# Kernel optimization log

Hardware: AMD Instinct MI355X
Metric: run time of the kernel (lower is better)

Reference implementation:

```python
import jax, jax.numpy as jnp
import numpy as np

V, C, E = 100000, 50000, 1250000
VF, CF, H = 32, 32, 64
ROUNDS = 3


def setup_inputs() -> dict:
    key = jax.random.key(0)
    ks = jax.random.split(key, 16)
    s = lambda d: 1.0 / np.sqrt(d)
    inp = {
        "var_feat": jax.random.normal(ks[0], (V, VF), dtype=jnp.float32),
        "constr_feat": jax.random.normal(ks[1], (C, CF), dtype=jnp.float32),
        "W_var": jax.random.uniform(ks[2], (VF, H), jnp.float32, -s(VF), s(VF)),
        "b_var": jax.random.uniform(ks[3], (H,), jnp.float32, -s(VF), s(VF)),
        "W_con": jax.random.uniform(ks[4], (CF, H), jnp.float32, -s(CF), s(CF)),
        "b_con": jax.random.uniform(ks[5], (H,), jnp.float32, -s(CF), s(CF)),
        "W_v2c": jax.random.uniform(ks[6], (H, H), jnp.float32, -s(H), s(H)),
        "b_v2c": jax.random.uniform(ks[7], (H,), jnp.float32, -s(H), s(H)),
        "W_c2v": jax.random.uniform(ks[8], (H, H), jnp.float32, -s(H), s(H)),
        "b_c2v": jax.random.uniform(ks[9], (H,), jnp.float32, -s(H), s(H)),
        "W_score": jax.random.uniform(ks[10], (H, 1), jnp.float32, -s(H), s(H)),
        "b_score": jax.random.uniform(ks[11], (1,), jnp.float32, -s(H), s(H)),
        "var_idx": jax.random.randint(ks[12], (E,), 0, V, dtype=jnp.int64 if jax.config.jax_enable_x64 else jnp.int32),
        "constr_idx": jax.random.randint(ks[13], (E,), 0, C, dtype=jnp.int64 if jax.config.jax_enable_x64 else jnp.int32),
    }
    return inp


def reference(var_feat, constr_feat, W_var, b_var, W_con, b_con, W_v2c, b_v2c,
              W_c2v, b_c2v, W_score, b_score, var_idx, constr_idx):
    nV = var_feat.shape[0]
    nC = constr_feat.shape[0]
    h_var = jax.nn.relu(var_feat @ W_var + b_var)          # [V, H]
    h_constr = jax.nn.relu(constr_feat @ W_con + b_con)    # [C, H]
    for _ in range(ROUNDS):
        # gather var states along edges, scatter-add into constraint buffer
        msg_c = jax.ops.segment_sum(h_var[var_idx], constr_idx, num_segments=nC)  # [C, H]
        h_constr = jax.nn.relu(h_constr + msg_c @ W_v2c + b_v2c)
        # gather constraint states along edges, scatter-add into variable buffer
        msg_v = jax.ops.segment_sum(h_constr[constr_idx], var_idx, num_segments=nV)  # [V, H]
        h_var = jax.nn.relu(h_var + msg_v @ W_c2v + b_c2v)
    scores = (h_var @ W_score + b_score).reshape(-1)       # [V]
    return scores
```

## Files before the change

kernel.cpp:

```cpp
#include <hip/hip_runtime.h>

typedef unsigned short u16;
typedef unsigned int u32;
typedef __attribute__((ext_vector_type(8))) short short8v;
typedef __attribute__((ext_vector_type(4))) float f32x4;

#define V_N 100000
#define C_N 50000
#define E_N 1250000
#define VF_N 32
#define H_N 64
#define ROUNDS 3

#define TILE 4096
#define NT ((E_N + TILE - 1) / TILE)
#define NB_C ((C_N + 127) / 128)
#define NB_V ((V_N + 255) / 256)
#define FC_BLOCKS 768
#define KPAD 72

static __device__ __forceinline__ float bf2f(u16 x) {
  return __uint_as_float(((u32)x) << 16);
}
static __device__ __forceinline__ u16 f2bf(float f) {
  u32 u = __float_as_uint(f);
  u32 r = (u + 0x7fff + ((u >> 16) & 1)) >> 16;
  return (u16)r;
}


__global__ __launch_bounds__(256) void bucket_hist(const int* __restrict__ vi,
                                                   const int* __restrict__ ci,
                                                   int* __restrict__ gh_c,
                                                   int* __restrict__ gh_v) {
  __shared__ int hc[NB_C], hv[NB_V];
  int t = threadIdx.x;
  for (int j = t; j < NB_C; j += 256) hc[j] = 0;
  for (int j = t; j < NB_V; j += 256) hv[j] = 0;
  __syncthreads();
  int base = blockIdx.x * TILE;
#pragma unroll
  for (int i = 0; i < 16; ++i) {
    int idx = base + i * 256 + t;
    if (idx < E_N) {
      atomicAdd(&hc[ci[idx] >> 7], 1);
      atomicAdd(&hv[vi[idx] >> 8], 1);
    }
  }
  __syncthreads();
  for (int j = t; j < NB_C; j += 256) if (hc[j]) atomicAdd(&gh_c[j], hc[j]);
  for (int j = t; j < NB_V; j += 256) if (hv[j]) atomicAdd(&gh_v[j], hv[j]);
}

__global__ __launch_bounds__(512) void bucket_scan(const int* __restrict__ gh_c,
                                                   const int* __restrict__ gh_v,
                                                   int* __restrict__ base_c,
                                                   int* __restrict__ cursor_c,
                                                   int* __restrict__ base_v,
                                                   int* __restrict__ cursor_v,
                                                   int* __restrict__ rs_c,
                                                   int* __restrict__ rs_v) {
  __shared__ int lds[512];
  int t = threadIdx.x;
  int x = (t < NB_C) ? gh_c[t] : 0;
  lds[t] = x;
  __syncthreads();
  for (int off = 1; off < 512; off <<= 1) {
    int v = (t >= off) ? lds[t - off] : 0;
    __syncthreads();
    lds[t] += v;
    __syncthreads();
  }
  int excl = lds[t] - x;
  if (t < NB_C) { base_c[t] = excl; cursor_c[t] = excl; }
  if (t == 511) base_c[NB_C] = lds[511];
  __syncthreads();
  int y = (t < NB_V) ? gh_v[t] : 0;
  lds[t] = y;
  __syncthreads();
  for (int off = 1; off < 512; off <<= 1) {
    int v = (t >= off) ? lds[t - off] : 0;
    __syncthreads();
    lds[t] += v;
    __syncthreads();
  }
  int excl2 = lds[t] - y;
  if (t < NB_V) { base_v[t] = excl2; cursor_v[t] = excl2; }
  if (t == 511) base_v[NB_V] = lds[511];
  if (t == 0) { rs_c[C_N] = E_N; rs_v[V_N] = E_N; }
}

__global__ __launch_bounds__(256) void scatter_pack(const int* __restrict__ vi,
                                                    const int* __restrict__ ci,
                                                    int* __restrict__ cursor_c,
                                                    int* __restrict__ cursor_v,
                                                    int* __restrict__ packed_c,
                                                    int* __restrict__ packed_v) {
  __shared__ int hc[NB_C], hv[NB_V], sc[NB_C], sv[NB_V];
  int t = threadIdx.x;
  for (int j = t; j < NB_C; j += 256) hc[j] = 0;
  for (int j = t; j < NB_V; j += 256) hv[j] = 0;
  __syncthreads();
  int base = blockIdx.x * TILE;
  int cc[16], vv[16];
#pragma unroll
  for (int i = 0; i < 16; ++i) {
    int idx = base + i * 256 + t;
    if (idx < E_N) {
      cc[i] = ci[idx];
      vv[i] = vi[idx];
      atomicAdd(&hc[cc[i] >> 7], 1);
      atomicAdd(&hv[vv[i] >> 8], 1);
    } else {
      cc[i] = -1;
      vv[i] = -1;
    }
  }
  __syncthreads();
  for (int j = t; j < NB_C; j += 256) {
    int n = hc[j];
    if (n > 0) sc[j] = atomicAdd(&cursor_c[j], n);
    hc[j] = 0;
  }
  for (int j = t; j < NB_V; j += 256) {
    int n = hv[j];
    if (n > 0) sv[j] = atomicAdd(&cursor_v[j], n);
    hv[j] = 0;
  }
  __syncthreads();
#pragma unroll
  for (int i = 0; i < 16; ++i) {
    if (cc[i] >= 0) {
      int b = cc[i] >> 7;
      int r = atomicAdd(&hc[b], 1);
      packed_c[sc[b] + r] = ((cc[i] & 127) << 17) | vv[i];
      int b2 = vv[i] >> 8;
      int r2 = atomicAdd(&hv[b2], 1);
      packed_v[sv[b2] + r2] = ((vv[i] & 255) << 17) | cc[i];
    }
  }
}

template <int LOCAL_N, int N_DEST>
__global__ __launch_bounds__(256) void fine_sort(const int* __restrict__ packed,
                                                 const int* __restrict__ base,
                                                 int* __restrict__ rs,
                                                 int* __restrict__ srco) {
  __shared__ int cnt[LOCAL_N];
  __shared__ int excl[LOCAL_N];
  int b = blockIdx.x, t = threadIdx.x;
  int s0 = base[b], s1 = base[b + 1];
  if (t < LOCAL_N) cnt[t] = 0;
  __syncthreads();
  for (int i = s0 + t; i < s1; i += 256) atomicAdd(&cnt[packed[i] >> 17], 1);
  __syncthreads();
  if (t == 0) {
    int run = 0;
    for (int k = 0; k < LOCAL_N; ++k) { excl[k] = run; run += cnt[k]; }
  }
  __syncthreads();
  if (t < LOCAL_N) {
    int d = b * LOCAL_N + t;
    if (d < N_DEST) rs[d] = s0 + excl[t];
    cnt[t] = excl[t];
  }
  __syncthreads();
  for (int i = s0 + t; i < s1; i += 256) {
    int w = packed[i];
    int ld = w >> 17;
    int pos = s0 + atomicAdd(&cnt[ld], 1);
    srco[pos] = w & 0x1FFFF;
  }
}


__global__ __launch_bounds__(256) void prep_w(const float* __restrict__ W1,
                                              const float* __restrict__ W2,
                                              u16* __restrict__ wp) {
  int i = blockIdx.x * 256 + threadIdx.x;
  if (i >= H_N * H_N) return;
  int k = i >> 6, n = i & 63;
  float w1 = W1[i];
  u16 h1 = f2bf(w1);
  u16 l1 = f2bf(w1 - bf2f(h1));
  wp[(0 * 64 + n) * 64 + k] = h1;
  wp[(1 * 64 + n) * 64 + k] = l1;
  float w2 = W2[i];
  u16 h2 = f2bf(w2);
  u16 l2 = f2bf(w2 - bf2f(h2));
  wp[(2 * 64 + n) * 64 + k] = h2;
  wp[(3 * 64 + n) * 64 + k] = l2;
}


template <int WRITE_BF>
__global__ __launch_bounds__(256) void init_mlp(const float* __restrict__ feat,
                                                const float* __restrict__ W,
                                                const float* __restrict__ b,
                                                float* __restrict__ h,
                                                u16* __restrict__ hbf, int n) {
  __shared__ float Wl[VF_N * H_N];
  for (int i = threadIdx.x; i < VF_N * H_N; i += 256) Wl[i] = W[i];
  __syncthreads();
  int g = (blockIdx.x * 256 + threadIdx.x) >> 4;
  int lane = threadIdx.x & 15;
  if (g >= n) return;
  float2 rv = *(const float2*)&feat[(size_t)g * VF_N + lane * 2];
  float4 acc = *(const float4*)&b[lane * 4];
#pragma unroll
  for (int k = 0; k < VF_N; ++k) {
    float el = (k & 1) ? rv.y : rv.x;
    float v = __shfl(el, k >> 1, 16);
    float4 w = *(const float4*)&Wl[k * H_N + lane * 4];
    acc.x += v * w.x; acc.y += v * w.y; acc.z += v * w.z; acc.w += v * w.w;
  }
  acc.x = fmaxf(acc.x, 0.f); acc.y = fmaxf(acc.y, 0.f);
  acc.z = fmaxf(acc.z, 0.f); acc.w = fmaxf(acc.w, 0.f);
  *(float4*)&h[(size_t)g * H_N + lane * 4] = acc;
  if (WRITE_BF) {
    ushort4 q;
    q.x = f2bf(acc.x); q.y = f2bf(acc.y); q.z = f2bf(acc.z); q.w = f2bf(acc.w);
    *(ushort4*)&hbf[(size_t)g * H_N + lane * 4] = q;
  }
}


static __device__ __forceinline__ void gather_rows_bf16(const u16* __restrict__ tbl,
                                                        const int* __restrict__ src,
                                                        int s, int e, int lane,
                                                        float4& acc) {
  int p = s;
  for (; p + 16 <= e; p += 16) {
    int myidx = src[p + lane];
    ushort4 vv[16];
#pragma unroll
    for (int j = 0; j < 16; ++j) {
      int sj = __shfl(myidx, j, 16);
      vv[j] = *(const ushort4*)&tbl[(size_t)sj * H_N + lane * 4];
    }
#pragma unroll
    for (int j = 0; j < 16; ++j) {
      acc.x += bf2f(vv[j].x); acc.y += bf2f(vv[j].y);
      acc.z += bf2f(vv[j].z); acc.w += bf2f(vv[j].w);
    }
  }
  if (p < e) {
    int cnt = e - p;
    int myidx = (lane < cnt) ? src[p + lane] : 0;
    ushort4 vv[16];
#pragma unroll
    for (int j = 0; j < 16; ++j) {
      int sj = __shfl(myidx, j, 16);
      vv[j] = *(const ushort4*)&tbl[(size_t)sj * H_N + lane * 4];
    }
#pragma unroll
    for (int j = 0; j < 16; ++j) {
      if (j < cnt) {
        acc.x += bf2f(vv[j].x); acc.y += bf2f(vv[j].y);
        acc.z += bf2f(vv[j].z); acc.w += bf2f(vv[j].w);
      }
    }
  }
}


__global__ __launch_bounds__(256) void fused_c(const u16* __restrict__ h_var_bf,
                                               const int* __restrict__ rs,
                                               const int* __restrict__ src,
                                               const u16* __restrict__ wp,
                                               const float* __restrict__ b1g,
                                               float* __restrict__ h_con,
                                               u16* __restrict__ t_out) {
  __shared__ u16 Wlds[4 * 64 * 64];
  __shared__ u16 Aplanes[4][2 * 16 * KPAD];

  for (int i = threadIdx.x; i < 4 * 64 * 64 / 2; i += 256)
    ((u32*)Wlds)[i] = ((const u32*)wp)[i];
  __syncthreads();

  int lane64 = threadIdx.x & 63;
  int wave = threadIdx.x >> 6;
  int lane = threadIdx.x & 15;
  int grp = (threadIdx.x >> 4) & 3;
  int arow = lane64 & 15;
  int kq = lane64 >> 4;
  u16* P = &Aplanes[wave][0];

  float bias[4];
#pragma unroll
  for (int nt = 0; nt < 4; ++nt) bias[nt] = b1g[nt * 16 + arow];

  for (int base = (blockIdx.x * 4 + wave) * 16; base < C_N;
       base += FC_BLOCKS * 4 * 16) {
    for (int q = 0; q < 4; ++q) {
      int row = 4 * q + grp;
      int g = base + row;
      float4 acc = {0.f, 0.f, 0.f, 0.f};
      if (g < C_N) gather_rows_bf16(h_var_bf, src, rs[g], rs[g + 1], lane, acc);
      ushort4 qh, ql;
      qh.x = f2bf(acc.x); ql.x = f2bf(acc.x - bf2f(qh.x));
      qh.y = f2bf(acc.y); ql.y = f2bf(acc.y - bf2f(qh.y));
      qh.z = f2bf(acc.z); ql.z = f2bf(acc.z - bf2f(qh.z));
      qh.w = f2bf(acc.w); ql.w = f2bf(acc.w - bf2f(qh.w));
      *(ushort4*)&P[0 * 16 * KPAD + row * KPAD + lane * 4] = qh;
      *(ushort4*)&P[1 * 16 * KPAD + row * KPAD + lane * 4] = ql;
    }
    asm volatile("" ::: "memory");
    short8v A1h[2], A1l[2];
#pragma unroll
    for (int ks = 0; ks < 2; ++ks) {
      A1h[ks] = *(const short8v*)&P[0 * 16 * KPAD + arow * KPAD + ks * 32 + kq * 8];
      A1l[ks] = *(const short8v*)&P[1 * 16 * KPAD + arow * KPAD + ks * 32 + kq * 8];
    }
    asm volatile("" ::: "memory");
#pragma unroll
    for (int nt = 0; nt < 4; ++nt) {
      int bcol = nt * 16 + arow;
      f32x4 c = {0.f, 0.f, 0.f, 0.f};
#pragma unroll
      for (int ks = 0; ks < 2; ++ks) {
        short8v Bh = *(const short8v*)&Wlds[(0 * 64 + bcol) * 64 + ks * 32 + kq * 8];
        short8v Bl = *(const short8v*)&Wlds[(1 * 64 + bcol) * 64 + ks * 32 + kq * 8];
        c = __builtin_amdgcn_mfma_f32_16x16x32_bf16(A1h[ks], Bh, c, 0, 0, 0);
        c = __builtin_amdgcn_mfma_f32_16x16x32_bf16(A1l[ks], Bh, c, 0, 0, 0);
        c = __builtin_amdgcn_mfma_f32_16x16x32_bf16(A1h[ks], Bl, c, 0, 0, 0);
      }
#pragma unroll
      for (int r = 0; r < 4; ++r) {
        int row = kq * 4 + r;
        int g = base + row;
        float hv = (g < C_N) ? h_con[(size_t)g * H_N + nt * 16 + arow] : 0.f;
        float hn = fmaxf(hv + c[r] + bias[nt], 0.f);
        if (g < C_N) h_con[(size_t)g * H_N + nt * 16 + arow] = hn;
        u16 hi = f2bf(hn);
        u16 lo = f2bf(hn - bf2f(hi));
        P[0 * 16 * KPAD + row * KPAD + nt * 16 + arow] = hi;
        P[1 * 16 * KPAD + row * KPAD + nt * 16 + arow] = lo;
      }
    }
    asm volatile("" ::: "memory");
    short8v A2h[2], A2l[2];
#pragma unroll
    for (int ks = 0; ks < 2; ++ks) {
      A2h[ks] = *(const short8v*)&P[0 * 16 * KPAD + arow * KPAD + ks * 32 + kq * 8];
      A2l[ks] = *(const short8v*)&P[1 * 16 * KPAD + arow * KPAD + ks * 32 + kq * 8];
    }
    asm volatile("" ::: "memory");
#pragma unroll
    for (int nt = 0; nt < 4; ++nt) {
      int bcol = nt * 16 + arow;
      f32x4 c = {0.f, 0.f, 0.f, 0.f};
#pragma unroll
      for (int ks = 0; ks < 2; ++ks) {
        short8v Bh = *(const short8v*)&Wlds[(2 * 64 + bcol) * 64 + ks * 32 + kq * 8];
        short8v Bl = *(const short8v*)&Wlds[(3 * 64 + bcol) * 64 + ks * 32 + kq * 8];
        c = __builtin_amdgcn_mfma_f32_16x16x32_bf16(A2h[ks], Bh, c, 0, 0, 0);
        c = __builtin_amdgcn_mfma_f32_16x16x32_bf16(A2l[ks], Bh, c, 0, 0, 0);
        c = __builtin_amdgcn_mfma_f32_16x16x32_bf16(A2h[ks], Bl, c, 0, 0, 0);
      }
#pragma unroll
      for (int r = 0; r < 4; ++r) {
        int row = kq * 4 + r;
        int g = base + row;
        if (g < C_N) t_out[(size_t)g * H_N + nt * 16 + arow] = f2bf(c[r]);
      }
    }
    asm volatile("" ::: "memory");
  }
}


template <int DO_SCORE>
__global__ __launch_bounds__(256) void gather_v_k(const u16* __restrict__ t,
                                                  const int* __restrict__ rs,
                                                  const int* __restrict__ src,
                                                  const float* __restrict__ bias,
                                                  float* __restrict__ h,
                                                  u16* __restrict__ hbf,
                                                  const float* __restrict__ Ws,
                                                  const float* __restrict__ bs,
                                                  float* __restrict__ out) {
  int g = (blockIdx.x * 256 + threadIdx.x) >> 4;
  int lane = threadIdx.x & 15;
  if (g >= V_N) return;
  int s = rs[g], e = rs[g + 1];
  float4 acc = {0.f, 0.f, 0.f, 0.f};
  gather_rows_bf16(t, src, s, e, lane, acc);
  float4 hv = *(const float4*)&h[(size_t)g * H_N + lane * 4];
  float4 b4 = *(const float4*)&bias[lane * 4];
  float4 hn;
  hn.x = fmaxf(hv.x + acc.x + b4.x, 0.f);
  hn.y = fmaxf(hv.y + acc.y + b4.y, 0.f);
  hn.z = fmaxf(hv.z + acc.z + b4.z, 0.f);
  hn.w = fmaxf(hv.w + acc.w + b4.w, 0.f);
  if (DO_SCORE) {
    float4 w = *(const float4*)&Ws[lane * 4];
    float d = hn.x * w.x + hn.y * w.y + hn.z * w.z + hn.w * w.w;
    d += __shfl_down(d, 8, 16);
    d += __shfl_down(d, 4, 16);
    d += __shfl_down(d, 2, 16);
    d += __shfl_down(d, 1, 16);
    if (lane == 0) out[g] = d + bs[0];
  } else {
    *(float4*)&h[(size_t)g * H_N + lane * 4] = hn;
    ushort4 q;
    q.x = f2bf(hn.x); q.y = f2bf(hn.y); q.z = f2bf(hn.z); q.w = f2bf(hn.w);
    *(ushort4*)&hbf[(size_t)g * H_N + lane * 4] = q;
  }
}


extern "C" void kernel_launch(void* const* d_in, const int* in_sizes, int n_in,
                              void* d_out, int out_size, void* d_ws, size_t ws_size,
                              hipStream_t stream) {
  const float* var_feat = (const float*)d_in[0];
  const float* con_feat = (const float*)d_in[1];
  const float* W_var = (const float*)d_in[2];
  const float* b_var = (const float*)d_in[3];
  const float* W_con = (const float*)d_in[4];
  const float* b_con = (const float*)d_in[5];
  const float* W_v2c = (const float*)d_in[6];
  const float* b_v2c = (const float*)d_in[7];
  const float* W_c2v = (const float*)d_in[8];
  const float* b_c2v = (const float*)d_in[9];
  const float* W_score = (const float*)d_in[10];
  const float* b_score = (const float*)d_in[11];
  const int* var_idx = (const int*)d_in[12];
  const int* constr_idx = (const int*)d_in[13];
  float* out = (float*)d_out;

  char* p = (char*)d_ws;
  auto alloc = [&](size_t bytes) {
    char* r = p;
    p += (bytes + 255) & ~(size_t)255;
    return r;
  };
  float* h_var = (float*)alloc((size_t)V_N * H_N * 4);
  u16* h_var_bf = (u16*)alloc((size_t)V_N * H_N * 2);
  float* h_con = (float*)alloc((size_t)C_N * H_N * 4);
  u16* t_bf = (u16*)alloc((size_t)C_N * H_N * 2);
  u16* wp = (u16*)alloc((size_t)4 * 64 * 64 * 2);
  int* rs_c = (int*)alloc((size_t)(C_N + 1) * 4);
  int* rs_v = (int*)alloc((size_t)(V_N + 1) * 4);
  int* src_c = (int*)alloc((size_t)E_N * 4);
  int* src_v = (int*)alloc((size_t)E_N * 4);
  int* packed_c = (int*)alloc((size_t)E_N * 4);
  int* packed_v = (int*)alloc((size_t)E_N * 4);
  int* ghist_c = (int*)alloc((size_t)NB_C * 4);
  int* ghist_v = (int*)alloc((size_t)NB_V * 4);
  int* base_c = (int*)alloc((size_t)(NB_C + 1) * 4);
  int* base_v = (int*)alloc((size_t)(NB_V + 1) * 4);
  int* cursor_c = (int*)alloc((size_t)NB_C * 4);
  int* cursor_v = (int*)alloc((size_t)NB_V * 4);

  hipMemsetAsync(ghist_c, 0, (size_t)NB_C * 4, stream);
  hipMemsetAsync(ghist_v, 0, (size_t)NB_V * 4, stream);

  bucket_hist<<<NT, 256, 0, stream>>>(var_idx, constr_idx, ghist_c, ghist_v);
  bucket_scan<<<1, 512, 0, stream>>>(ghist_c, ghist_v, base_c, cursor_c,
                                     base_v, cursor_v, rs_c, rs_v);
  scatter_pack<<<NT, 256, 0, stream>>>(var_idx, constr_idx, cursor_c, cursor_v,
                                       packed_c, packed_v);
  fine_sort<128, C_N><<<NB_C, 256, 0, stream>>>(packed_c, base_c, rs_c, src_c);
  fine_sort<256, V_N><<<NB_V, 256, 0, stream>>>(packed_v, base_v, rs_v, src_v);

  prep_w<<<(H_N * H_N + 255) / 256, 256, 0, stream>>>(W_v2c, W_c2v, wp);

  init_mlp<1><<<(V_N + 15) / 16, 256, 0, stream>>>(var_feat, W_var, b_var, h_var, h_var_bf, V_N);
  init_mlp<0><<<(C_N + 15) / 16, 256, 0, stream>>>(con_feat, W_con, b_con, h_con, nullptr, C_N);

  for (int r = 0; r < ROUNDS; ++r) {
    fused_c<<<FC_BLOCKS, 256, 0, stream>>>(h_var_bf, rs_c, src_c, wp,
                                           b_v2c, h_con, t_bf);
    if (r < ROUNDS - 1) {
      gather_v_k<0><<<(V_N + 15) / 16, 256, 0, stream>>>(t_bf, rs_v, src_v, b_c2v, h_var,
                                                         h_var_bf, nullptr, nullptr, nullptr);
    } else {
      gather_v_k<1><<<(V_N + 15) / 16, 256, 0, stream>>>(t_bf, rs_v, src_v, b_c2v, h_var,
                                                         nullptr, W_score, b_score, out);
    }
  }
}
```

Before: 345.2 us.

## Use 16-byte edge gathers and atomic tile scheduling in fused_c

The constraint-side gather now has each 16-lane group fetch two edge rows at once using 16-byte (8 bf16) loads per lane, and the two half-sums are combined with a shuffle. Each wave also takes 16-row tiles from a global atomic counter, one counter per round, instead of a static stride, which balances the uneven edge counts across waves. This gives wider memory transactions and better load balance, at the cost of more registers for the 16 short8 loads and one atomic per tile.

```diff
diff --git a/kernel.cpp b/kernel.cpp
--- a/kernel.cpp
+++ b/kernel.cpp
@@ -18,6 +18,7 @@
 #define NB_V ((V_N + 255) / 256)
 #define FC_BLOCKS 768
 #define KPAD 72
+#define NTILES_C ((C_N + 15) / 16)
 
 static __device__ __forceinline__ float bf2f(u16 x) {
   return __uint_as_float(((u32)x) << 16);
@@ -264,13 +265,47 @@
 }
 
 
+static __device__ __forceinline__ void gather_rows_wide(const u16* __restrict__ tbl,
+                                                        const int* __restrict__ src,
+                                                        int s, int e, int lane,
+                                                        float* acc8) {
+  int half = lane >> 3;
+  int oct = lane & 7;
+  int p = s;
+  for (; p < e; p += 32) {
+    int rem = e - p;
+    int i0 = p + lane, i1 = p + 16 + lane;
+    int s0 = (i0 < e) ? src[i0] : 0;
+    int s1 = (i1 < e) ? src[i1] : 0;
+    short8v vv[16];
+#pragma unroll
+    for (int j = 0; j < 16; ++j) {
+      int re = 2 * j;
+      int ro = 2 * j + 1;
+      int idA = __shfl((re >= 16) ? s1 : s0, re & 15, 16);
+      int idB = __shfl((ro >= 16) ? s1 : s0, ro & 15, 16);
+      int id = half ? idB : idA;
+      vv[j] = *(const short8v*)&tbl[(size_t)id * H_N + oct * 8];
+    }
+#pragma unroll
+    for (int j = 0; j < 16; ++j) {
+      if (2 * j + half < rem) {
+#pragma unroll
+        for (int k = 0; k < 8; ++k) acc8[k] += bf2f((u16)vv[j][k]);
+      }
+    }
+  }
+}
+
+
 __global__ __launch_bounds__(256) void fused_c(const u16* __restrict__ h_var_bf,
                                                const int* __restrict__ rs,
                                                const int* __restrict__ src,
                                                const u16* __restrict__ wp,
                                                const float* __restrict__ b1g,
                                                float* __restrict__ h_con,
-                                               u16* __restrict__ t_out) {
+                                               u16* __restrict__ t_out,
+                                               int* __restrict__ tile_ctr) {
   __shared__ u16 Wlds[4 * 64 * 64];
   __shared__ u16 Aplanes[4][2 * 16 * KPAD];
 
@@ -282,6 +317,8 @@
   int wave = threadIdx.x >> 6;
   int lane = threadIdx.x & 15;
   int grp = (threadIdx.x >> 4) & 3;
+  int half = lane >> 3;
+  int oct = lane & 7;
   int arow = lane64 & 15;
   int kq = lane64 >> 4;
   u16* P = &Aplanes[wave][0];
@@ -290,20 +327,30 @@
 #pragma unroll
   for (int nt = 0; nt < 4; ++nt) bias[nt] = b1g[nt * 16 + arow];
 
-  for (int base = (blockIdx.x * 4 + wave) * 16; base < C_N;
-       base += FC_BLOCKS * 4 * 16) {
+  for (;;) {
+    int tile = 0;
+    if (lane64 == 0) tile = atomicAdd(tile_ctr, 1);
+    tile = __shfl(tile, 0, 64);
+    if (tile >= NTILES_C) break;
+    int base = tile * 16;
     for (int q = 0; q < 4; ++q) {
       int row = 4 * q + grp;
       int g = base + row;
-      float4 acc = {0.f, 0.f, 0.f, 0.f};
-      if (g < C_N) gather_rows_bf16(h_var_bf, src, rs[g], rs[g + 1], lane, acc);
-      ushort4 qh, ql;
-      qh.x = f2bf(acc.x); ql.x = f2bf(acc.x - bf2f(qh.x));
-      qh.y = f2bf(acc.y); ql.y = f2bf(acc.y - bf2f(qh.y));
-      qh.z = f2bf(acc.z); ql.z = f2bf(acc.z - bf2f(qh.z));
-      qh.w = f2bf(acc.w); ql.w = f2bf(acc.w - bf2f(qh.w));
-      *(ushort4*)&P[0 * 16 * KPAD + row * KPAD + lane * 4] = qh;
-      *(ushort4*)&P[1 * 16 * KPAD + row * KPAD + lane * 4] = ql;
+      float acc8[8] = {0.f, 0.f, 0.f, 0.f, 0.f, 0.f, 0.f, 0.f};
+      if (g < C_N) gather_rows_wide(h_var_bf, src, rs[g], rs[g + 1], lane, acc8);
+      short8v hi8, lo8;
+#pragma unroll
+      for (int k = 0; k < 8; ++k) {
+        float full = acc8[k] + __shfl_xor(acc8[k], 8, 16);
+        u16 h = f2bf(full);
+        u16 l = f2bf(full - bf2f(h));
+        hi8[k] = (short)h;
+        lo8[k] = (short)l;
+      }
+      if (half == 0) {
+        *(short8v*)&P[0 * 16 * KPAD + row * KPAD + oct * 8] = hi8;
+        *(short8v*)&P[1 * 16 * KPAD + row * KPAD + oct * 8] = lo8;
+      }
     }
     asm volatile("" ::: "memory");
     short8v A1h[2], A1l[2];
@@ -452,9 +499,11 @@
   int* base_v = (int*)alloc((size_t)(NB_V + 1) * 4);
   int* cursor_c = (int*)alloc((size_t)NB_C * 4);
   int* cursor_v = (int*)alloc((size_t)NB_V * 4);
+  int* tile_ctr = (int*)alloc((size_t)ROUNDS * 4);
 
   hipMemsetAsync(ghist_c, 0, (size_t)NB_C * 4, stream);
   hipMemsetAsync(ghist_v, 0, (size_t)NB_V * 4, stream);
+  hipMemsetAsync(tile_ctr, 0, (size_t)ROUNDS * 4, stream);
 
   bucket_hist<<<NT, 256, 0, stream>>>(var_idx, constr_idx, ghist_c, ghist_v);
   bucket_scan<<<1, 512, 0, stream>>>(ghist_c, ghist_v, base_c, cursor_c,
@@ -471,7 +520,7 @@
 
   for (int r = 0; r < ROUNDS; ++r) {
     fused_c<<<FC_BLOCKS, 256, 0, stream>>>(h_var_bf, rs_c, src_c, wp,
-                                           b_v2c, h_con, t_bf);
+                                           b_v2c, h_con, t_bf, &tile_ctr[r]);
     if (r < ROUNDS - 1) {
       gather_v_k<0><<<(V_N + 15) / 16, 256, 0, stream>>>(t_bf, rs_v, src_v, b_c2v, h_var,
                                                          h_var_bf, nullptr, nullptr, nullptr);
```

Result: slower. 470.1 us (+36.2%).

## Use one tile per wave with 8-wave blocks in fused constraint kernel

Applied to the files above, without the earlier changes.

Replaces the persistent grid-stride loop in fused_c with one 16-row tile per wave, 8 waves per 512-thread block, and a grid sized to cover all tiles. The four row gathers are issued before any conversion so their loads can overlap. The hi and lo bf16 planes now share one LDS buffer per wave and are built one after the other, which halves per-wave LDS for the A planes. This trades the amortized weight-to-LDS load of persistent blocks for more blocks, each reloading the 32KB of weights, in exchange for better load balance and occupancy.

```diff
diff --git a/kernel.cpp b/kernel.cpp
--- a/kernel.cpp
+++ b/kernel.cpp
@@ -16,8 +16,10 @@
 #define NT ((E_N + TILE - 1) / TILE)
 #define NB_C ((C_N + 127) / 128)
 #define NB_V ((V_N + 255) / 256)
-#define FC_BLOCKS 768
 #define KPAD 72
+#define NTILES_C ((C_N + 15) / 16)
+#define FC_WAVES 8
+#define FC_BLOCKS ((NTILES_C + FC_WAVES - 1) / FC_WAVES)
 
 static __device__ __forceinline__ float bf2f(u16 x) {
   return __uint_as_float(((u32)x) << 16);
@@ -264,7 +266,7 @@
 }
 
 
-__global__ __launch_bounds__(256) void fused_c(const u16* __restrict__ h_var_bf,
+__global__ __launch_bounds__(512) void fused_c(const u16* __restrict__ h_var_bf,
                                                const int* __restrict__ rs,
                                                const int* __restrict__ src,
                                                const u16* __restrict__ wp,
@@ -272,9 +274,9 @@
                                                float* __restrict__ h_con,
                                                u16* __restrict__ t_out) {
   __shared__ u16 Wlds[4 * 64 * 64];
-  __shared__ u16 Aplanes[4][2 * 16 * KPAD];
-
-  for (int i = threadIdx.x; i < 4 * 64 * 64 / 2; i += 256)
+  __shared__ u16 Aplane[FC_WAVES][16 * KPAD];
+
+  for (int i = threadIdx.x; i < 4 * 64 * 64 / 2; i += 512)
     ((u32*)Wlds)[i] = ((const u32*)wp)[i];
   __syncthreads();
 
@@ -284,88 +286,120 @@
   int grp = (threadIdx.x >> 4) & 3;
   int arow = lane64 & 15;
   int kq = lane64 >> 4;
-  u16* P = &Aplanes[wave][0];
+  u16* P = &Aplane[wave][0];
+
+  int tile = blockIdx.x * FC_WAVES + wave;
+  if (tile >= NTILES_C) return;
+  int base = tile * 16;
 
   float bias[4];
 #pragma unroll
   for (int nt = 0; nt < 4; ++nt) bias[nt] = b1g[nt * 16 + arow];
 
-  for (int base = (blockIdx.x * 4 + wave) * 16; base < C_N;
-       base += FC_BLOCKS * 4 * 16) {
-    for (int q = 0; q < 4; ++q) {
-      int row = 4 * q + grp;
+  float4 accs[4];
+#pragma unroll
+  for (int q = 0; q < 4; ++q) {
+    int row = 4 * q + grp;
+    int g = base + row;
+    float4 a = {0.f, 0.f, 0.f, 0.f};
+    if (g < C_N) gather_rows_bf16(h_var_bf, src, rs[g], rs[g + 1], lane, a);
+    accs[q] = a;
+  }
+#pragma unroll
+  for (int q = 0; q < 4; ++q) {
+    int row = 4 * q + grp;
+    ushort4 qh;
+    qh.x = f2bf(accs[q].x); qh.y = f2bf(accs[q].y);
+    qh.z = f2bf(accs[q].z); qh.w = f2bf(accs[q].w);
+    *(ushort4*)&P[row * KPAD + lane * 4] = qh;
+  }
+  asm volatile("" ::: "memory");
+  short8v A1h[2];
+#pragma unroll
+  for (int ks = 0; ks < 2; ++ks)
+    A1h[ks] = *(const short8v*)&P[arow * KPAD + ks * 32 + kq * 8];
+  asm volatile("" ::: "memory");
+#pragma unroll
+  for (int q = 0; q < 4; ++q) {
+    int row = 4 * q + grp;
+    ushort4 ql;
+    ql.x = f2bf(accs[q].x - bf2f(f2bf(accs[q].x)));
+    ql.y = f2bf(accs[q].y - bf2f(f2bf(accs[q].y)));
+    ql.z = f2bf(accs[q].z - bf2f(f2bf(accs[q].z)));
+    ql.w = f2bf(accs[q].w - bf2f(f2bf(accs[q].w)));
+    *(ushort4*)&P[row * KPAD + lane * 4] = ql;
+  }
+  asm volatile("" ::: "memory");
+  short8v A1l[2];
+#pragma unroll
+  for (int ks = 0; ks < 2; ++ks)
+    A1l[ks] = *(const short8v*)&P[arow * KPAD + ks * 32 + kq * 8];
+  asm volatile("" ::: "memory");
+  float hn[4][4];
+#pragma unroll
+  for (int nt = 0; nt < 4; ++nt) {
+    int bcol = nt * 16 + arow;
+    f32x4 c = {0.f, 0.f, 0.f, 0.f};
+#pragma unroll
+    for (int ks = 0; ks < 2; ++ks) {
+      short8v Bh = *(const short8v*)&Wlds[(0 * 64 + bcol) * 64 + ks * 32 + kq * 8];
+      short8v Bl = *(const short8v*)&Wlds[(1 * 64 + bcol) * 64 + ks * 32 + kq * 8];
+      c = __builtin_amdgcn_mfma_f32_16x16x32_bf16(A1h[ks], Bh, c, 0, 0, 0);
+      c = __builtin_amdgcn_mfma_f32_16x16x32_bf16(A1l[ks], Bh, c, 0, 0, 0);
+      c = __builtin_amdgcn_mfma_f32_16x16x32_bf16(A1h[ks], Bl, c, 0, 0, 0);
+    }
+#pragma unroll
+    for (int r = 0; r < 4; ++r) {
+      int row = kq * 4 + r;
       int g = base + row;
-      float4 acc = {0.f, 0.f, 0.f, 0.f};
-      if (g < C_N) gather_rows_bf16(h_var_bf, src, rs[g], rs[g + 1], lane, acc);
-      ushort4 qh, ql;
-      qh.x = f2bf(acc.x); ql.x = f2bf(acc.x - bf2f(qh.x));
-      qh.y = f2bf(acc.y); ql.y = f2bf(acc.y - bf2f(qh.y));
-      qh.z = f2bf(acc.z); ql.z = f2bf(acc.z - bf2f(qh.z));
-      qh.w = f2bf(acc.w); ql.w = f2bf(acc.w - bf2f(qh.w));
-      *(ushort4*)&P[0 * 16 * KPAD + row * KPAD + lane * 4] = qh;
-      *(ushort4*)&P[1 * 16 * KPAD + row * KPAD + lane * 4] = ql;
-    }
-    asm volatile("" ::: "memory");
-    short8v A1h[2], A1l[2];
+      float hv = (g < C_N) ? h_con[(size_t)g * H_N + nt * 16 + arow] : 0.f;
+      float v = fmaxf(hv + c[r] + bias[nt], 0.f);
+      if (g < C_N) h_con[(size_t)g * H_N + nt * 16 + arow] = v;
+      hn[nt][r] = v;
+    }
+  }
+#pragma unroll
+  for (int nt = 0; nt < 4; ++nt)
+#pragma unroll
+    for (int r = 0; r < 4; ++r)
+      P[(kq * 4 + r) * KPAD + nt * 16 + arow] = f2bf(hn[nt][r]);
+  asm volatile("" ::: "memory");
+  short8v A2h[2];
+#pragma unroll
+  for (int ks = 0; ks < 2; ++ks)
+    A2h[ks] = *(const short8v*)&P[arow * KPAD + ks * 32 + kq * 8];
+  asm volatile("" ::: "memory");
+#pragma unroll
+  for (int nt = 0; nt < 4; ++nt)
+#pragma unroll
+    for (int r = 0; r < 4; ++r) {
+      u16 hi = f2bf(hn[nt][r]);
+      P[(kq * 4 + r) * KPAD + nt * 16 + arow] = f2bf(hn[nt][r] - bf2f(hi));
+    }
+  asm volatile("" ::: "memory");
+  short8v A2l[2];
+#pragma unroll
+  for (int ks = 0; ks < 2; ++ks)
+    A2l[ks] = *(const short8v*)&P[arow * KPAD + ks * 32 + kq * 8];
+  asm volatile("" ::: "memory");
+#pragma unroll
+  for (int nt = 0; nt < 4; ++nt) {
+    int bcol = nt * 16 + arow;
+    f32x4 c = {0.f, 0.f, 0.f, 0.f};
 #pragma unroll
     for (int ks = 0; ks < 2; ++ks) {
-      A1h[ks] = *(const short8v*)&P[0 * 16 * KPAD + arow * KPAD + ks * 32 + kq * 8];
-      A1l[ks] = *(const short8v*)&P[1 * 16 * KPAD + arow * KPAD + ks * 32 + kq * 8];
-    }
-    asm volatile("" ::: "memory");
-#pragma unroll
-    for (int nt = 0; nt < 4; ++nt) {
-      int bcol = nt * 16 + arow;
-      f32x4 c = {0.f, 0.f, 0.f, 0.f};
-#pragma unroll
-      for (int ks = 0; ks < 2; ++ks) {
-        short8v Bh = *(const short8v*)&Wlds[(0 * 64 + bcol) * 64 + ks * 32 + kq * 8];
-        short8v Bl = *(const short8v*)&Wlds[(1 * 64 + bcol) * 64 + ks * 32 + kq * 8];
-        c = __builtin_amdgcn_mfma_f32_16x16x32_bf16(A1h[ks], Bh, c, 0, 0, 0);
-        c = __builtin_amdgcn_mfma_f32_16x16x32_bf16(A1l[ks], Bh, c, 0, 0, 0);
-        c = __builtin_amdgcn_mfma_f32_16x16x32_bf16(A1h[ks], Bl, c, 0, 0, 0);
-      }
-#pragma unroll
-      for (int r = 0; r < 4; ++r) {
-        int row = kq * 4 + r;
-        int g = base + row;
-        float hv = (g < C_N) ? h_con[(size_t)g * H_N + nt * 16 + arow] : 0.f;
-        float hn = fmaxf(hv + c[r] + bias[nt], 0.f);
-        if (g < C_N) h_con[(size_t)g * H_N + nt * 16 + arow] = hn;
-        u16 hi = f2bf(hn);
-        u16 lo = f2bf(hn - bf2f(hi));
-        P[0 * 16 * KPAD + row * KPAD + nt * 16 + arow] = hi;
-        P[1 * 16 * KPAD + row * KPAD + nt * 16 + arow] = lo;
-      }
-    }
-    asm volatile("" ::: "memory");
-    short8v A2h[2], A2l[2];
-#pragma unroll
-    for (int ks = 0; ks < 2; ++ks) {
-      A2h[ks] = *(const short8v*)&P[0 * 16 * KPAD + arow * KPAD + ks * 32 + kq * 8];
-      A2l[ks] = *(const short8v*)&P[1 * 16 * KPAD + arow * KPAD + ks * 32 + kq * 8];
-    }
-    asm volatile("" ::: "memory");
-#pragma unroll
-    for (int nt = 0; nt < 4; ++nt) {
-      int bcol = nt * 16 + arow;
-      f32x4 c = {0.f, 0.f, 0.f, 0.f};
-#pragma unroll
-      for (int ks = 0; ks < 2; ++ks) {
-        short8v Bh = *(const short8v*)&Wlds[(2 * 64 + bcol) * 64 + ks * 32 + kq * 8];
-        short8v Bl = *(const short8v*)&Wlds[(3 * 64 + bcol) * 64 + ks * 32 + kq * 8];
-        c = __builtin_amdgcn_mfma_f32_16x16x32_bf16(A2h[ks], Bh, c, 0, 0, 0);
-        c = __builtin_amdgcn_mfma_f32_16x16x32_bf16(A2l[ks], Bh, c, 0, 0, 0);
-        c = __builtin_amdgcn_mfma_f32_16x16x32_bf16(A2h[ks], Bl, c, 0, 0, 0);
-      }
-#pragma unroll
-      for (int r = 0; r < 4; ++r) {
-        int row = kq * 4 + r;
-        int g = base + row;
-        if (g < C_N) t_out[(size_t)g * H_N + nt * 16 + arow] = f2bf(c[r]);
-      }
-    }
-    asm volatile("" ::: "memory");
+      short8v Bh = *(const short8v*)&Wlds[(2 * 64 + bcol) * 64 + ks * 32 + kq * 8];
+      short8v Bl = *(const short8v*)&Wlds[(3 * 64 + bcol) * 64 + ks * 32 + kq * 8];
+      c = __builtin_amdgcn_mfma_f32_16x16x32_bf16(A2h[ks], Bh, c, 0, 0, 0);
+      c = __builtin_amdgcn_mfma_f32_16x16x32_bf16(A2l[ks], Bh, c, 0, 0, 0);
+      c = __builtin_amdgcn_mfma_f32_16x16x32_bf16(A2h[ks], Bl, c, 0, 0, 0);
+    }
+#pragma unroll
+    for (int r = 0; r < 4; ++r) {
+      int row = kq * 4 + r;
+      int g = base + row;
+      if (g < C_N) t_out[(size_t)g * H_N + nt * 16 + arow] = f2bf(c[r]);
+    }
   }
 }
 
@@ -470,7 +504,7 @@
   init_mlp<0><<<(C_N + 15) / 16, 256, 0, stream>>>(con_feat, W_con, b_con, h_con, nullptr, C_N);
 
   for (int r = 0; r < ROUNDS; ++r) {
-    fused_c<<<FC_BLOCKS, 256, 0, stream>>>(h_var_bf, rs_c, src_c, wp,
+    fused_c<<<FC_BLOCKS, 512, 0, stream>>>(h_var_bf, rs_c, src_c, wp,
                                            b_v2c, h_con, t_bf);
     if (r < ROUNDS - 1) {
       gather_v_k<0><<<(V_N + 15) / 16, 256, 0, stream>>>(t_bf, rs_v, src_v, b_c2v, h_var,
```

Result: faster. 296.3 us (-14.2%).
